# Kernel tuning notes

Hardware: AMD Instinct MI355X
Metric: run time of the kernel (lower is better)

Reference implementation:

```python
import jax, jax.numpy as jnp
import numpy as np

B, T = 32, 48
INPUT_DIM = 40000
TRAJ = 10
H = 256
OUT = 40000
TD = 48
L = 2
E = 128
DIN = E + TD  # 176


def setup_inputs() -> dict:
    key = jax.random.key(0)
    ks = jax.random.split(key, 16)
    s = 0.05
    inp = {
        "locations": jax.random.randint(ks[0], (B, T), 0, INPUT_DIM),
        "times": jax.random.randint(ks[1], (B, T), 0, TD),
        "labels": jax.random.randint(ks[2], (B,), 0, TRAJ),
        "embed_table": jax.random.normal(ks[3], (INPUT_DIM, E), dtype=jnp.float32) * s,
        "traj_table": jax.random.normal(ks[4], (TRAJ, H * L), dtype=jnp.float32) * s,
        "fc_w": jax.random.normal(ks[5], (OUT + TD, H), dtype=jnp.float32) * s,
        "fc_b": jnp.zeros((OUT + TD,), dtype=jnp.float32),
        "w_ih0": jax.random.normal(ks[6], (3 * H, DIN), dtype=jnp.float32) * s,
        "w_hh0": jax.random.normal(ks[7], (3 * H, H), dtype=jnp.float32) * s,
        "b_ih0": jnp.zeros((3 * H,), dtype=jnp.float32),
        "b_hh0": jnp.zeros((3 * H,), dtype=jnp.float32),
        "w_ih1": jax.random.normal(ks[8], (3 * H, H), dtype=jnp.float32) * s,
        "w_hh1": jax.random.normal(ks[9], (3 * H, H), dtype=jnp.float32) * s,
        "b_ih1": jnp.zeros((3 * H,), dtype=jnp.float32),
        "b_hh1": jnp.zeros((3 * H,), dtype=jnp.float32),
    }
    return inp


def gru_layer(x, h0, w_ih, w_hh, b_ih, b_hh):
    """PyTorch-semantics GRU layer. x: [T,B,din], h0: [B,H] -> [T,B,H]."""
    # precompute input projections for all timesteps (gates ordered r,z,n)
    xp = jnp.einsum('tbd,gd->tbg', x, w_ih) + b_ih  # [T,B,3H]

    def step(h, xp_t):
        hp = h @ w_hh.T + b_hh                      # [B,3H]
        xr, xz, xn = jnp.split(xp_t, 3, axis=-1)
        hr, hz, hn = jnp.split(hp, 3, axis=-1)
        r = jax.nn.sigmoid(xr + hr)
        z = jax.nn.sigmoid(xz + hz)
        n = jnp.tanh(xn + r * hn)
        h_new = (1.0 - z) * n + z * h
        return h_new, h_new

    _, ys = jax.lax.scan(step, h0, xp)
    return ys


def reference(locations, times, labels, embed_table, traj_table, fc_w, fc_b,
              w_ih0, w_hh0, b_ih0, b_hh0, w_ih1, w_hh1, b_ih1, b_hh1):
    x = embed_table[locations]                                  # [B,T,E]
    th = jax.nn.one_hot(times, TD, dtype=x.dtype)               # [B,T,TD]
    x = jnp.concatenate([x, th], axis=-1).transpose(1, 0, 2)    # [T,B,E+TD]
    # init_hidden: view (B, L*H) -> (L, -1, H), a raw reshape as in torch
    h0 = traj_table[labels].reshape(L, -1, H)                   # [L,B,H]
    y = gru_layer(x, h0[0], w_ih0, w_hh0, b_ih0, b_hh0)
    y = gru_layer(y, h0[1], w_ih1, w_hh1, b_ih1, b_hh1)         # [T,B,H]
    out = jax.nn.relu(y).transpose(1, 0, 2) @ fc_w.T + fc_b     # [B,T,OUT+TD]
    loc = jax.nn.log_softmax(out[..., :OUT], axis=-1)
    tm = jax.nn.log_softmax(out[..., OUT:], axis=-1)
    return loc, tm
```

## Files before the change

### kernel.cpp

```cpp
#include <hip/hip_runtime.h>
#include <hip/hip_cooperative_groups.h>
#include <math.h>

namespace cg = cooperative_groups;

typedef __attribute__((ext_vector_type(4))) float f32x4;
typedef __attribute__((ext_vector_type(8))) short s16x8;

constexpr int B = 32, T = 48, H = 256, E = 128, TD = 48;
constexpr int OUT = 40000, NOUTC = 40048, NPADC = 40064;
constexpr int G3 = 768, DIN = 176;

__device__ __forceinline__ float sigmoidf_(float x){ return 1.f/(1.f+__expf(-x)); }
__device__ __forceinline__ float tanhf_(float x){
  float e = __expf(2.f*x);
  return 1.f - 2.f/(e + 1.f);
}
__device__ __forceinline__ unsigned short f2bf(float f){
  unsigned int u = __float_as_uint(f);
  u += 0x7fffu + ((u>>16)&1u);
  return (unsigned short)(u>>16);
}
__device__ __forceinline__ s16x8 pack8(float4 u, float4 v){
  s16x8 r;
  r[0]=(short)f2bf(u.x); r[1]=(short)f2bf(u.y); r[2]=(short)f2bf(u.z); r[3]=(short)f2bf(u.w);
  r[4]=(short)f2bf(v.x); r[5]=(short)f2bf(v.y); r[6]=(short)f2bf(v.z); r[7]=(short)f2bf(v.w);
  return r;
}
__device__ __forceinline__ void gl_lds16(const unsigned short* g, unsigned short* l){
  __builtin_amdgcn_global_load_lds((const __attribute__((address_space(1))) void*)g,
                                   (__attribute__((address_space(3))) void*)l, 16, 0, 0);
}

__global__ void wt_kernel(const float* __restrict__ w_ih0, float* __restrict__ wT){
  int i = blockIdx.x*256 + threadIdx.x;
  if (i >= E*G3) return;
  int e = i / G3, g = i % G3;
  wT[i] = w_ih0[g*DIN + e];
}

__global__ void xp0_kernel(const int* __restrict__ locations, const int* __restrict__ times,
                           const float* __restrict__ embed, const float* __restrict__ wT,
                           const float* __restrict__ w_ih0, const float* __restrict__ b_ih0,
                           float* __restrict__ xp0)
{
  __shared__ float emb_s[16][E];
  __shared__ int tm_s[16];
  const int r0 = blockIdx.x * 16;
  const int tid = threadIdx.x;
  for (int i = tid; i < 16*E; i += 256) {
    int p = i >> 7, e = i & 127;
    int r = r0 + p; int t = r >> 5, b = r & 31;
    emb_s[p][e] = embed[(size_t)locations[b*T + t]*E + e];
  }
  if (tid < 16) {
    int r = r0 + tid; int t = r >> 5, b = r & 31;
    tm_s[tid] = times[b*T + t];
  }
  __syncthreads();
  const int g = tid;
  float acc[16][3];
  #pragma unroll
  for (int p=0;p<16;p++){acc[p][0]=0.f;acc[p][1]=0.f;acc[p][2]=0.f;}
  for (int e = 0; e < E; e += 4) {
    float w0_[4], w1_[4], w2_[4];
    #pragma unroll
    for (int i=0;i<4;i++){
      w0_[i]=wT[(e+i)*G3 + g];
      w1_[i]=wT[(e+i)*G3 + 256 + g];
      w2_[i]=wT[(e+i)*G3 + 512 + g];
    }
    #pragma unroll
    for (int p=0;p<16;p++){
      float4 ev = *(const float4*)&emb_s[p][e];
      acc[p][0] += ev.x*w0_[0]+ev.y*w0_[1]+ev.z*w0_[2]+ev.w*w0_[3];
      acc[p][1] += ev.x*w1_[0]+ev.y*w1_[1]+ev.z*w1_[2]+ev.w*w1_[3];
      acc[p][2] += ev.x*w2_[0]+ev.y*w2_[1]+ev.z*w2_[2]+ev.w*w2_[3];
    }
  }
  #pragma unroll
  for (int p=0;p<16;p++){
    int r = r0+p; int tt = tm_s[p];
    xp0[(size_t)r*G3 + g]       = acc[p][0] + b_ih0[g]     + w_ih0[g*DIN       + E + tt];
    xp0[(size_t)r*G3 + 256 + g] = acc[p][1] + b_ih0[g+256] + w_ih0[(g+256)*DIN + E + tt];
    xp0[(size_t)r*G3 + 512 + g] = acc[p][2] + b_ih0[g+512] + w_ih0[(g+512)*DIN + E + tt];
  }
}

struct GruArgs {
  const float* xp0; const float* traj; const int* labels;
  const float* w_hh0; const float* b_hh0;
  const float* w_ih1; const float* w_hh1; const float* b_ih1; const float* b_hh1;
  float* h0f; float* h1f;
  unsigned short* h0bf; unsigned short* h1bf;
  unsigned short* abf;
};

__global__ void __launch_bounds__(384, 2) gru_kernel(GruArgs a)
{
  __shared__ unsigned short A0[32*264];
  __shared__ unsigned short A1[32*264];
  __shared__ float gl0[3*32*17];
  __shared__ float gl1[4*32*17];
  cg::grid_group grid = cg::this_grid();
  const int tid  = threadIdx.x;
  const int jt   = blockIdx.x;
  const int wv   = tid >> 6;
  const int lane = tid & 63;
  const int g    = wv % 3, mt = wv / 3;
  const int fn   = lane & 15;
  const int fq   = lane >> 4;

  const int row = g*256 + jt*16 + fn;
  s16x8 b0[8], b1[16];
  #pragma unroll
  for (int kk = 0; kk < 8; ++kk) {
    const float* p0 = a.w_hh0 + (size_t)row*H + kk*32 + fq*8;
    const float* p1 = a.w_ih1 + (size_t)row*H + kk*32 + fq*8;
    const float* p2 = a.w_hh1 + (size_t)row*H + kk*32 + fq*8;
    b0[kk]    = pack8(*(const float4*)p0, *(const float4*)(p0+4));
    b1[kk]    = pack8(*(const float4*)p1, *(const float4*)(p1+4));
    b1[kk+8]  = pack8(*(const float4*)p2, *(const float4*)(p2+4));
  }

  for (int i = blockIdx.x*384 + tid; i < 2*B*H; i += 16*384) {
    int l = i >> 13, bb = (i >> 8) & 31, h = i & 255;
    float v = a.traj[(size_t)a.labels[l*16 + (bb>>1)]*512 + (bb&1)*256 + h];
    if (l == 0) { a.h0f[bb*256+h] = v;        a.h0bf[bb*256+h] = f2bf(v); }
    else        { a.h1f[8192+bb*256+h] = v;   a.h1bf[8192+bb*256+h] = f2bf(v); }
  }
  grid.sync();

  for (int p = 0; p <= T; ++p) {
    const int cur = p & 1, nxt = cur ^ 1;
    {
      const unsigned short* s0 = a.h0bf + cur*8192;
      const unsigned short* s1 = a.h1bf + cur*8192;
      for (int i = tid; i < 1024; i += 384) {
        int b = i >> 5, kg = (i & 31) * 8;
        *(uint4*)&A0[b*264 + kg] = *(const uint4*)&s0[b*256 + kg];
        *(uint4*)&A1[b*264 + kg] = *(const uint4*)&s1[b*256 + kg];
      }
    }
    __syncthreads();

    if (p < T) {
      f32x4 acc = (f32x4){0.f,0.f,0.f,0.f};
      #pragma unroll
      for (int kk = 0; kk < 8; ++kk) {
        s16x8 af = *(const s16x8*)&A0[(mt*16 + fn)*264 + kk*32 + fq*8];
        acc = __builtin_amdgcn_mfma_f32_16x16x32_bf16(af, b0[kk], acc, 0, 0, 0);
      }
      #pragma unroll
      for (int i = 0; i < 4; ++i)
        gl0[(g*32 + mt*16 + fq*4 + i)*17 + fn] = acc[i];
    }
    if (p >= 1) {
      if (g < 2) {
        f32x4 acc = (f32x4){0.f,0.f,0.f,0.f};
        #pragma unroll
        for (int kk = 0; kk < 8; ++kk) {
          s16x8 af = *(const s16x8*)&A0[(mt*16 + fn)*264 + kk*32 + fq*8];
          acc = __builtin_amdgcn_mfma_f32_16x16x32_bf16(af, b1[kk], acc, 0, 0, 0);
        }
        #pragma unroll
        for (int kk = 0; kk < 8; ++kk) {
          s16x8 af = *(const s16x8*)&A1[(mt*16 + fn)*264 + kk*32 + fq*8];
          acc = __builtin_amdgcn_mfma_f32_16x16x32_bf16(af, b1[8+kk], acc, 0, 0, 0);
        }
        #pragma unroll
        for (int i = 0; i < 4; ++i)
          gl1[(g*32 + mt*16 + fq*4 + i)*17 + fn] = acc[i];
      } else {
        f32x4 ax = (f32x4){0.f,0.f,0.f,0.f}, ah = (f32x4){0.f,0.f,0.f,0.f};
        #pragma unroll
        for (int kk = 0; kk < 8; ++kk) {
          s16x8 afx = *(const s16x8*)&A0[(mt*16 + fn)*264 + kk*32 + fq*8];
          s16x8 afh = *(const s16x8*)&A1[(mt*16 + fn)*264 + kk*32 + fq*8];
          ax = __builtin_amdgcn_mfma_f32_16x16x32_bf16(afx, b1[kk],   ax, 0, 0, 0);
          ah = __builtin_amdgcn_mfma_f32_16x16x32_bf16(afh, b1[8+kk], ah, 0, 0, 0);
        }
        #pragma unroll
        for (int i = 0; i < 4; ++i) {
          gl1[(2*32 + mt*16 + fq*4 + i)*17 + fn] = ax[i];
          gl1[(3*32 + mt*16 + fq*4 + i)*17 + fn] = ah[i];
        }
      }
    }
    __syncthreads();

    if (p < T) {
      for (int s = tid; s < 512; s += 384) {
        int b = s >> 4, j = s & 15, gj = jt*16 + j;
        float hr = gl0[(b)*17+j], hz = gl0[(32+b)*17+j], hn = gl0[(64+b)*17+j];
        const float* xp = a.xp0 + (size_t)(p*B + b)*G3 + gj;
        float xr = xp[0], xz = xp[256], xn = xp[512];
        float r = sigmoidf_(xr + hr + a.b_hh0[gj]);
        float z = sigmoidf_(xz + hz + a.b_hh0[256+gj]);
        float n = tanhf_(xn + r*(hn + a.b_hh0[512+gj]));
        float hp = a.h0f[cur*8192 + b*256 + gj];
        float hnew = (1.f - z)*n + z*hp;
        a.h0f [nxt*8192 + b*256 + gj] = hnew;
        a.h0bf[nxt*8192 + b*256 + gj] = f2bf(hnew);
      }
    }
    if (p >= 1) {
      const int t1 = p - 1;
      for (int s = tid; s < 512; s += 384) {
        int b = s >> 4, j = s & 15, gj = jt*16 + j;
        float gr = gl1[(b)*17+j],    gz = gl1[(32+b)*17+j];
        float nx = gl1[(64+b)*17+j], nh = gl1[(96+b)*17+j];
        float r = sigmoidf_(gr + a.b_ih1[gj]     + a.b_hh1[gj]);
        float z = sigmoidf_(gz + a.b_ih1[256+gj] + a.b_hh1[256+gj]);
        float n = tanhf_(nx + a.b_ih1[512+gj] + r*(nh + a.b_hh1[512+gj]));
        float hp = a.h1f[cur*8192 + b*256 + gj];
        float hnew = (1.f - z)*n + z*hp;
        a.h1f [nxt*8192 + b*256 + gj] = hnew;
        a.h1bf[nxt*8192 + b*256 + gj] = f2bf(hnew);
        a.abf[(size_t)(b*T + t1)*H + gj] = f2bf(fmaxf(hnew, 0.f));
      }
    }
    grid.sync();
  }
}

__global__ void castw_kernel(const float* __restrict__ fcw, unsigned short* __restrict__ wbf){
  int g = blockIdx.x*256 + threadIdx.x;
  if (g >= NPADC*64) return;
  int row = g >> 6;
  ushort4 o;
  if (row < NOUTC) {
    float4 v = ((const float4*)fcw)[g];
    o.x=f2bf(v.x); o.y=f2bf(v.y); o.z=f2bf(v.z); o.w=f2bf(v.w);
  } else { o.x=0; o.y=0; o.z=0; o.w=0; }
  ((ushort4*)wbf)[g] = o;
}

__global__ void __launch_bounds__(256) gemm_kernel(const unsigned short* __restrict__ Abf,
                                                   const unsigned short* __restrict__ Wbf,
                                                   const float* __restrict__ fc_b,
                                                   float* __restrict__ dout)
{
  __shared__ unsigned short As[128*32];
  __shared__ unsigned short Ws[128*32];
  const int m0 = blockIdx.x * 128;
  const int n0 = blockIdx.y * 128;
  const int tid = threadIdx.x;
  const int lane = tid & 63;
  const int wv = tid >> 6;
  f32x4 acc[2][8];
  #pragma unroll
  for (int i=0;i<2;i++)
    #pragma unroll
    for(int jx=0;jx<8;jx++) acc[i][jx] = (f32x4){0.f,0.f,0.f,0.f};

  const int srow = tid >> 2;
  const int skoff = (tid & 3) * 8;
  const unsigned short* aptr = Abf + (size_t)(m0 + srow)*256 + skoff;
  const unsigned short* wptr = Wbf + (size_t)(n0 + srow)*256 + skoff;
  unsigned short* asd = &As[tid*8];
  unsigned short* wsd = &Ws[tid*8];

  const int fr = lane & 15;
  const int fk = (lane >> 4) * 8;

  for (int kk = 0; kk < 256; kk += 32) {
    gl_lds16(aptr + kk,            asd);
    gl_lds16(aptr + 64*256 + kk,   asd + 64*32);
    gl_lds16(wptr + kk,            wsd);
    gl_lds16(wptr + 64*256 + kk,   wsd + 64*32);
    __syncthreads();
    s16x8 a0 = *(const s16x8*)&As[(wv*32 + fr)*32 + fk];
    s16x8 a1 = *(const s16x8*)&As[(wv*32 + 16 + fr)*32 + fk];
    #pragma unroll
    for (int ct = 0; ct < 8; ++ct) {
      s16x8 bfr = *(const s16x8*)&Ws[(ct*16 + fr)*32 + fk];
      acc[0][ct] = __builtin_amdgcn_mfma_f32_16x16x32_bf16(a0, bfr, acc[0][ct], 0, 0, 0);
      acc[1][ct] = __builtin_amdgcn_mfma_f32_16x16x32_bf16(a1, bfr, acc[1][ct], 0, 0, 0);
    }
    __syncthreads();
  }

  const int quad = lane >> 4;
  #pragma unroll
  for (int rt = 0; rt < 2; ++rt) {
    #pragma unroll
    for (int ct = 0; ct < 8; ++ct) {
      int col = n0 + ct*16 + fr;
      if (col < NOUTC) {
        float bias = fc_b[col];
        #pragma unroll
        for (int i = 0; i < 4; ++i) {
          int row = m0 + wv*32 + rt*16 + quad*4 + i;
          float v = acc[rt][ct][i] + bias;
          if (col < OUT) dout[(size_t)row*OUT + col] = v;
          else dout[(size_t)OUT*B*T + (size_t)row*TD + (col - OUT)] = v;
        }
      }
    }
  }
}

__global__ void stats_kernel(const float* __restrict__ dout, float* __restrict__ logz){
  const int r = blockIdx.x;
  const float4* row = (const float4*)(dout + (size_t)r*OUT);
  float m = -INFINITY, s = 0.f;
  for (int i = threadIdx.x; i < OUT/4; i += 256) {
    float4 v = row[i];
    float mx = fmaxf(fmaxf(v.x,v.y), fmaxf(v.z,v.w));
    if (mx > m) { s *= __expf(m - mx); m = mx; }
    s += __expf(v.x-m)+__expf(v.y-m)+__expf(v.z-m)+__expf(v.w-m);
  }
  #pragma unroll
  for (int off = 1; off < 64; off <<= 1) {
    float m2 = __shfl_xor(m, off);
    float s2 = __shfl_xor(s, off);
    float nm = fmaxf(m, m2);
    s = s*__expf(m-nm) + s2*__expf(m2-nm);
    m = nm;
  }
  __shared__ float sm[4], ss[4];
  if ((threadIdx.x & 63) == 0){ sm[threadIdx.x>>6]=m; ss[threadIdx.x>>6]=s; }
  __syncthreads();
  if (threadIdx.x == 0){
    float M=sm[0], S=ss[0];
    #pragma unroll
    for (int w=1;w<4;w++){
      float nm=fmaxf(M,sm[w]); S = S*__expf(M-nm)+ss[w]*__expf(sm[w]-nm); M=nm;
    }
    logz[r] = M + logf(S);
  }
}

__global__ void norm_kernel(float* __restrict__ dout, const float* __restrict__ logz){
  size_t i = (size_t)blockIdx.x*256 + threadIdx.x;
  if (i >= (size_t)B*T*OUT/4) return;
  int r = (int)(i / (OUT/4));
  float lz = logz[r];
  float4* p = (float4*)dout + i;
  float4 v = *p;
  v.x -= lz; v.y -= lz; v.z -= lz; v.w -= lz;
  *p = v;
}

__global__ void tm_kernel(float* __restrict__ dout){
  const int r = blockIdx.x;
  const int lane = threadIdx.x;
  float* base = dout + (size_t)OUT*B*T + (size_t)r*TD;
  float v = (lane < TD) ? base[lane] : -INFINITY;
  float m = v;
  #pragma unroll
  for (int off=32; off; off>>=1) m = fmaxf(m, __shfl_xor(m, off));
  float e = (lane < TD) ? __expf(v - m) : 0.f;
  float s = e;
  #pragma unroll
  for (int off=32; off; off>>=1) s += __shfl_xor(s, off);
  float lz = m + logf(s);
  if (lane < TD) base[lane] = v - lz;
}

extern "C" void kernel_launch(void* const* d_in, const int* in_sizes, int n_in,
                              void* d_out, int out_size, void* d_ws, size_t ws_size,
                              hipStream_t stream)
{
  const int*   locations = (const int*)d_in[0];
  const int*   times     = (const int*)d_in[1];
  const int*   labels    = (const int*)d_in[2];
  const float* embed     = (const float*)d_in[3];
  const float* traj      = (const float*)d_in[4];
  const float* fc_w      = (const float*)d_in[5];
  const float* fc_b      = (const float*)d_in[6];
  const float* w_ih0     = (const float*)d_in[7];
  const float* w_hh0     = (const float*)d_in[8];
  const float* b_ih0     = (const float*)d_in[9];
  const float* b_hh0     = (const float*)d_in[10];
  const float* w_ih1     = (const float*)d_in[11];
  const float* w_hh1     = (const float*)d_in[12];
  const float* b_ih1     = (const float*)d_in[13];
  const float* b_hh1     = (const float*)d_in[14];
  float* out = (float*)d_out;
  char* ws = (char*)d_ws;

  float* xp0            = (float*)(ws);
  float* h0f            = (float*)(ws + 4718592);
  float* h1f            = (float*)(ws + 4784128);
  unsigned short* h0bf  = (unsigned short*)(ws + 4849664);
  unsigned short* h1bf  = (unsigned short*)(ws + 4882432);
  float* logz           = (float*)(ws + 4915200);
  unsigned short* abf   = (unsigned short*)(ws + 4921344);
  unsigned short* wbf   = (unsigned short*)(ws + 5707776);
  float* wT             = (float*)(ws + 26220544);

  castw_kernel<<<dim3((NPADC*64 + 255)/256), dim3(256), 0, stream>>>(fc_w, wbf);
  wt_kernel<<<dim3((E*G3 + 255)/256), dim3(256), 0, stream>>>(w_ih0, wT);
  xp0_kernel<<<dim3(96), dim3(256), 0, stream>>>(locations, times, embed, wT, w_ih0, b_ih0, xp0);

  GruArgs ga{xp0, traj, labels, w_hh0, b_hh0, w_ih1, w_hh1, b_ih1, b_hh1,
             h0f, h1f, h0bf, h1bf, abf};
  void* kargs[] = { &ga };
  hipLaunchCooperativeKernel((void*)gru_kernel, dim3(16), dim3(384), kargs, 0, stream);

  gemm_kernel<<<dim3(12, 313), dim3(256), 0, stream>>>(abf, wbf, fc_b, out);
  stats_kernel<<<dim3(B*T), dim3(256), 0, stream>>>(out, logz);
  norm_kernel<<<dim3((B*T*OUT/4 + 255)/256), dim3(256), 0, stream>>>(out, logz);
  tm_kernel<<<dim3(B*T), dim3(64), 0, stream>>>(out);
}
```

Before: 892.7 us.

## Replace cooperative grid.sync with custom atomic barrier and LDS-resident GRU state

Replaces the cooperative-groups grid barrier in the recurrent GRU kernel with a hand-rolled monotonic atomic counter barrier, reset by an earlier kernel. It also keeps each block's fp32 hidden-state slice in shared memory and exchanges only packed bf16 state through a system-scope buffer, cutting per-step global traffic. The gate epilogue is reworked so each thread handles two adjacent columns. The spin-wait has an iteration cap that could silently break synchronization if a block is slow.

```diff
diff --git a/kernel.cpp b/kernel.cpp
--- a/kernel.cpp
+++ b/kernel.cpp
@@ -1,8 +1,5 @@
 #include <hip/hip_runtime.h>
-#include <hip/hip_cooperative_groups.h>
 #include <math.h>
-
-namespace cg = cooperative_groups;
 
 typedef __attribute__((ext_vector_type(4))) float f32x4;
 typedef __attribute__((ext_vector_type(8))) short s16x8;
@@ -31,9 +28,18 @@
   __builtin_amdgcn_global_load_lds((const __attribute__((address_space(1))) void*)g,
                                    (__attribute__((address_space(3))) void*)l, 16, 0, 0);
 }
-
-__global__ void wt_kernel(const float* __restrict__ w_ih0, float* __restrict__ wT){
+__device__ __forceinline__ void st_sc(unsigned* p, unsigned v){
+  __hip_atomic_store(p, v, __ATOMIC_RELAXED, __HIP_MEMORY_SCOPE_SYSTEM);
+}
+__device__ __forceinline__ unsigned long long ld_sc64(const unsigned long long* p){
+  return __hip_atomic_load(p, __ATOMIC_RELAXED, __HIP_MEMORY_SCOPE_SYSTEM);
+}
+
+__global__ void wt_kernel(const float* __restrict__ w_ih0, float* __restrict__ wT,
+                          unsigned* __restrict__ bar){
   int i = blockIdx.x*256 + threadIdx.x;
+  if (blockIdx.x == 0 && threadIdx.x == 0)
+    __hip_atomic_store(bar, 0u, __ATOMIC_RELAXED, __HIP_MEMORY_SCOPE_SYSTEM);
   if (i >= E*G3) return;
   int e = i / G3, g = i % G3;
   wT[i] = w_ih0[g*DIN + e];
@@ -91,18 +97,18 @@
   const float* xp0; const float* traj; const int* labels;
   const float* w_hh0; const float* b_hh0;
   const float* w_ih1; const float* w_hh1; const float* b_ih1; const float* b_hh1;
-  float* h0f; float* h1f;
-  unsigned short* h0bf; unsigned short* h1bf;
+  unsigned short* exch;
+  unsigned* bar;
   unsigned short* abf;
 };
 
 __global__ void __launch_bounds__(384, 2) gru_kernel(GruArgs a)
 {
-  __shared__ unsigned short A0[32*264];
-  __shared__ unsigned short A1[32*264];
+  __shared__ unsigned short Ash[2][32*264];
   __shared__ float gl0[3*32*17];
   __shared__ float gl1[4*32*17];
-  cg::grid_group grid = cg::this_grid();
+  __shared__ float hF0[512];
+  __shared__ float hF1[512];
   const int tid  = threadIdx.x;
   const int jt   = blockIdx.x;
   const int wv   = tid >> 6;
@@ -110,6 +116,7 @@
   const int g    = wv % 3, mt = wv / 3;
   const int fn   = lane & 15;
   const int fq   = lane >> 4;
+  unsigned* exch32 = (unsigned*)a.exch;
 
   const int row = g*256 + jt*16 + fn;
   s16x8 b0[8], b1[16];
@@ -123,23 +130,40 @@
     b1[kk+8]  = pack8(*(const float4*)p2, *(const float4*)(p2+4));
   }
 
-  for (int i = blockIdx.x*384 + tid; i < 2*B*H; i += 16*384) {
+  for (int i = tid; i < 2*B*H; i += 384) {
     int l = i >> 13, bb = (i >> 8) & 31, h = i & 255;
     float v = a.traj[(size_t)a.labels[l*16 + (bb>>1)]*512 + (bb&1)*256 + h];
-    if (l == 0) { a.h0f[bb*256+h] = v;        a.h0bf[bb*256+h] = f2bf(v); }
-    else        { a.h1f[8192+bb*256+h] = v;   a.h1bf[8192+bb*256+h] = f2bf(v); }
-  }
-  grid.sync();
+    Ash[l][bb*264 + h] = f2bf(v);
+  }
+  if (tid < 256) {
+    int b = tid >> 3, jp = tid & 7, j0 = jp*2, gj = jt*16 + j0;
+    float v00 = a.traj[(size_t)a.labels[(b>>1)]*512      + (b&1)*256 + gj];
+    float v01 = a.traj[(size_t)a.labels[(b>>1)]*512      + (b&1)*256 + gj+1];
+    float v10 = a.traj[(size_t)a.labels[16 + (b>>1)]*512 + (b&1)*256 + gj];
+    float v11 = a.traj[(size_t)a.labels[16 + (b>>1)]*512 + (b&1)*256 + gj+1];
+    hF0[b*16+j0] = v00; hF0[b*16+j0+1] = v01;
+    hF1[b*16+j0] = v10; hF1[b*16+j0+1] = v11;
+    st_sc(&exch32[(1*2+1)*4096 + b*128 + jt*8 + jp],
+          (unsigned)f2bf(v10) | ((unsigned)f2bf(v11) << 16));
+  }
 
   for (int p = 0; p <= T; ++p) {
     const int cur = p & 1, nxt = cur ^ 1;
-    {
-      const unsigned short* s0 = a.h0bf + cur*8192;
-      const unsigned short* s1 = a.h1bf + cur*8192;
-      for (int i = tid; i < 1024; i += 384) {
-        int b = i >> 5, kg = (i & 31) * 8;
-        *(uint4*)&A0[b*264 + kg] = *(const uint4*)&s0[b*256 + kg];
-        *(uint4*)&A1[b*264 + kg] = *(const uint4*)&s1[b*256 + kg];
+    if (p) {
+      const unsigned long long* src = (const unsigned long long*)a.exch + (size_t)cur*4096;
+      unsigned long long v[11];
+      #pragma unroll
+      for (int k = 0; k < 11; ++k) {
+        int i = tid + k*384;
+        if (i < 4096) v[k] = ld_sc64(&src[i]);
+      }
+      #pragma unroll
+      for (int k = 0; k < 11; ++k) {
+        int i = tid + k*384;
+        if (i < 4096) {
+          int st = i >> 11, bb = (i >> 6) & 31, k4 = (i & 63) << 2;
+          *(unsigned long long*)&Ash[st][bb*264 + k4] = v[k];
+        }
       }
     }
     __syncthreads();
@@ -148,7 +172,7 @@
       f32x4 acc = (f32x4){0.f,0.f,0.f,0.f};
       #pragma unroll
       for (int kk = 0; kk < 8; ++kk) {
-        s16x8 af = *(const s16x8*)&A0[(mt*16 + fn)*264 + kk*32 + fq*8];
+        s16x8 af = *(const s16x8*)&Ash[0][(mt*16 + fn)*264 + kk*32 + fq*8];
         acc = __builtin_amdgcn_mfma_f32_16x16x32_bf16(af, b0[kk], acc, 0, 0, 0);
       }
       #pragma unroll
@@ -160,12 +184,12 @@
         f32x4 acc = (f32x4){0.f,0.f,0.f,0.f};
         #pragma unroll
         for (int kk = 0; kk < 8; ++kk) {
-          s16x8 af = *(const s16x8*)&A0[(mt*16 + fn)*264 + kk*32 + fq*8];
+          s16x8 af = *(const s16x8*)&Ash[0][(mt*16 + fn)*264 + kk*32 + fq*8];
           acc = __builtin_amdgcn_mfma_f32_16x16x32_bf16(af, b1[kk], acc, 0, 0, 0);
         }
         #pragma unroll
         for (int kk = 0; kk < 8; ++kk) {
-          s16x8 af = *(const s16x8*)&A1[(mt*16 + fn)*264 + kk*32 + fq*8];
+          s16x8 af = *(const s16x8*)&Ash[1][(mt*16 + fn)*264 + kk*32 + fq*8];
           acc = __builtin_amdgcn_mfma_f32_16x16x32_bf16(af, b1[8+kk], acc, 0, 0, 0);
         }
         #pragma unroll
@@ -175,8 +199,8 @@
         f32x4 ax = (f32x4){0.f,0.f,0.f,0.f}, ah = (f32x4){0.f,0.f,0.f,0.f};
         #pragma unroll
         for (int kk = 0; kk < 8; ++kk) {
-          s16x8 afx = *(const s16x8*)&A0[(mt*16 + fn)*264 + kk*32 + fq*8];
-          s16x8 afh = *(const s16x8*)&A1[(mt*16 + fn)*264 + kk*32 + fq*8];
+          s16x8 afx = *(const s16x8*)&Ash[0][(mt*16 + fn)*264 + kk*32 + fq*8];
+          s16x8 afh = *(const s16x8*)&Ash[1][(mt*16 + fn)*264 + kk*32 + fq*8];
           ax = __builtin_amdgcn_mfma_f32_16x16x32_bf16(afx, b1[kk],   ax, 0, 0, 0);
           ah = __builtin_amdgcn_mfma_f32_16x16x32_bf16(afh, b1[8+kk], ah, 0, 0, 0);
         }
@@ -189,38 +213,54 @@
     }
     __syncthreads();
 
-    if (p < T) {
-      for (int s = tid; s < 512; s += 384) {
-        int b = s >> 4, j = s & 15, gj = jt*16 + j;
-        float hr = gl0[(b)*17+j], hz = gl0[(32+b)*17+j], hn = gl0[(64+b)*17+j];
+    if (tid < 256) {
+      const int b = tid >> 3, jp = tid & 7, j0 = jp*2, gj = jt*16 + j0;
+      if (p < T) {
         const float* xp = a.xp0 + (size_t)(p*B + b)*G3 + gj;
-        float xr = xp[0], xz = xp[256], xn = xp[512];
-        float r = sigmoidf_(xr + hr + a.b_hh0[gj]);
-        float z = sigmoidf_(xz + hz + a.b_hh0[256+gj]);
-        float n = tanhf_(xn + r*(hn + a.b_hh0[512+gj]));
-        float hp = a.h0f[cur*8192 + b*256 + gj];
-        float hnew = (1.f - z)*n + z*hp;
-        a.h0f [nxt*8192 + b*256 + gj] = hnew;
-        a.h0bf[nxt*8192 + b*256 + gj] = f2bf(hnew);
-      }
-    }
-    if (p >= 1) {
-      const int t1 = p - 1;
-      for (int s = tid; s < 512; s += 384) {
-        int b = s >> 4, j = s & 15, gj = jt*16 + j;
-        float gr = gl1[(b)*17+j],    gz = gl1[(32+b)*17+j];
-        float nx = gl1[(64+b)*17+j], nh = gl1[(96+b)*17+j];
-        float r = sigmoidf_(gr + a.b_ih1[gj]     + a.b_hh1[gj]);
-        float z = sigmoidf_(gz + a.b_ih1[256+gj] + a.b_hh1[256+gj]);
-        float n = tanhf_(nx + a.b_ih1[512+gj] + r*(nh + a.b_hh1[512+gj]));
-        float hp = a.h1f[cur*8192 + b*256 + gj];
-        float hnew = (1.f - z)*n + z*hp;
-        a.h1f [nxt*8192 + b*256 + gj] = hnew;
-        a.h1bf[nxt*8192 + b*256 + gj] = f2bf(hnew);
-        a.abf[(size_t)(b*T + t1)*H + gj] = f2bf(fmaxf(hnew, 0.f));
-      }
-    }
-    grid.sync();
+        float r0 = sigmoidf_(xp[0]   + gl0[(b)*17+j0]      + a.b_hh0[gj]);
+        float r1 = sigmoidf_(xp[1]   + gl0[(b)*17+j0+1]    + a.b_hh0[gj+1]);
+        float z0 = sigmoidf_(xp[256] + gl0[(32+b)*17+j0]   + a.b_hh0[256+gj]);
+        float z1 = sigmoidf_(xp[257] + gl0[(32+b)*17+j0+1] + a.b_hh0[256+gj+1]);
+        float n0 = tanhf_(xp[512] + r0*(gl0[(64+b)*17+j0]   + a.b_hh0[512+gj]));
+        float n1 = tanhf_(xp[513] + r1*(gl0[(64+b)*17+j0+1] + a.b_hh0[512+gj+1]));
+        float h0n = (1.f - z0)*n0 + z0*hF0[b*16+j0];
+        float h1n = (1.f - z1)*n1 + z1*hF0[b*16+j0+1];
+        hF0[b*16+j0] = h0n; hF0[b*16+j0+1] = h1n;
+        st_sc(&exch32[(nxt*2 + 0)*4096 + b*128 + jt*8 + jp],
+              (unsigned)f2bf(h0n) | ((unsigned)f2bf(h1n) << 16));
+      }
+      if (p >= 1) {
+        const int t1 = p - 1;
+        float r0 = sigmoidf_(gl1[(b)*17+j0]      + a.b_ih1[gj]     + a.b_hh1[gj]);
+        float r1 = sigmoidf_(gl1[(b)*17+j0+1]    + a.b_ih1[gj+1]   + a.b_hh1[gj+1]);
+        float z0 = sigmoidf_(gl1[(32+b)*17+j0]   + a.b_ih1[256+gj]   + a.b_hh1[256+gj]);
+        float z1 = sigmoidf_(gl1[(32+b)*17+j0+1] + a.b_ih1[256+gj+1] + a.b_hh1[256+gj+1]);
+        float n0 = tanhf_(gl1[(64+b)*17+j0]   + a.b_ih1[512+gj]
+                          + r0*(gl1[(96+b)*17+j0]   + a.b_hh1[512+gj]));
+        float n1 = tanhf_(gl1[(64+b)*17+j0+1] + a.b_ih1[512+gj+1]
+                          + r1*(gl1[(96+b)*17+j0+1] + a.b_hh1[512+gj+1]));
+        float h0n = (1.f - z0)*n0 + z0*hF1[b*16+j0];
+        float h1n = (1.f - z1)*n1 + z1*hF1[b*16+j0+1];
+        hF1[b*16+j0] = h0n; hF1[b*16+j0+1] = h1n;
+        st_sc(&exch32[(nxt*2 + 1)*4096 + b*128 + jt*8 + jp],
+              (unsigned)f2bf(h0n) | ((unsigned)f2bf(h1n) << 16));
+        ((unsigned*)a.abf)[((size_t)(b*T + t1)*H + gj) >> 1] =
+              (unsigned)f2bf(fmaxf(h0n,0.f)) | ((unsigned)f2bf(fmaxf(h1n,0.f)) << 16);
+      }
+    }
+    if (p == T) break;
+
+    asm volatile("s_waitcnt vmcnt(0)" ::: "memory");
+    __syncthreads();
+    if (tid == 0) {
+      __hip_atomic_fetch_add(a.bar, 1u, __ATOMIC_RELAXED, __HIP_MEMORY_SCOPE_SYSTEM);
+      const unsigned tgt = 16u*(unsigned)(p + 1);
+      unsigned it = 0;
+      while (__hip_atomic_load(a.bar, __ATOMIC_RELAXED, __HIP_MEMORY_SCOPE_SYSTEM) < tgt) {
+        if (++it > (1u<<21)) break;
+      }
+    }
+    __syncthreads();
   }
 }
 
@@ -382,21 +422,19 @@
   char* ws = (char*)d_ws;
 
   float* xp0            = (float*)(ws);
-  float* h0f            = (float*)(ws + 4718592);
-  float* h1f            = (float*)(ws + 4784128);
-  unsigned short* h0bf  = (unsigned short*)(ws + 4849664);
-  unsigned short* h1bf  = (unsigned short*)(ws + 4882432);
-  float* logz           = (float*)(ws + 4915200);
-  unsigned short* abf   = (unsigned short*)(ws + 4921344);
-  unsigned short* wbf   = (unsigned short*)(ws + 5707776);
-  float* wT             = (float*)(ws + 26220544);
+  unsigned short* exch  = (unsigned short*)(ws + 4718592);
+  unsigned* bar         = (unsigned*)(ws + 4784128);
+  float* logz           = (float*)(ws + 4784384);
+  unsigned short* abf   = (unsigned short*)(ws + 4790528);
+  unsigned short* wbf   = (unsigned short*)(ws + 5576960);
+  float* wT             = (float*)(ws + 26089728);
 
   castw_kernel<<<dim3((NPADC*64 + 255)/256), dim3(256), 0, stream>>>(fc_w, wbf);
-  wt_kernel<<<dim3((E*G3 + 255)/256), dim3(256), 0, stream>>>(w_ih0, wT);
+  wt_kernel<<<dim3((E*G3 + 255)/256), dim3(256), 0, stream>>>(w_ih0, wT, bar);
   xp0_kernel<<<dim3(96), dim3(256), 0, stream>>>(locations, times, embed, wT, w_ih0, b_ih0, xp0);
 
   GruArgs ga{xp0, traj, labels, w_hh0, b_hh0, w_ih1, w_hh1, b_ih1, b_hh1,
-             h0f, h1f, h0bf, h1bf, abf};
+             exch, bar, abf};
   void* kargs[] = { &ga };
   hipLaunchCooperativeKernel((void*)gru_kernel, dim3(16), dim3(384), kargs, 0, stream);
 
```

Result: faster. 772.0 us (-13.5%).
